# Performance work log

Measured on AMD Instinct MI355X. Metric: run time of the kernel, lower is better.

Reference implementation:

```python
import jax, jax.numpy as jnp
import numpy as np

B, L, DK, DV, H = 2, 2048, 512, 512, 8
DH_K = DK // H  # 64
DH_V = DV // H  # 64


def setup_inputs() -> dict:
    key = jax.random.key(0)
    ks = jax.random.split(key, 6)
    scale_w = 1.0 / np.sqrt(DK)
    return {
        "keys": jax.random.normal(ks[0], (B, L, DK), dtype=jnp.float32),
        "queries": jax.random.normal(ks[1], (B, L, DK), dtype=jnp.float32),
        "values": jax.random.normal(ks[2], (B, L, DV), dtype=jnp.float32),
        "WQ": jax.random.normal(ks[3], (H, DK, DH_K), dtype=jnp.float32) * scale_w,
        "WK": jax.random.normal(ks[4], (H, DK, DH_K), dtype=jnp.float32) * scale_w,
        "WV": jax.random.normal(ks[5], (H, DV, DH_V), dtype=jnp.float32) * scale_w,
    }


def reference(keys, queries, values, WQ, WK, WV):
    # Per-head projections, vectorized over all H heads at once.
    Q = jnp.einsum('bld,hde->bhle', queries, WQ)   # [B,H,Lq,dh]
    K = jnp.einsum('bld,hde->bhle', keys, WK)      # [B,H,Lk,dh]
    V = jnp.einsum('bld,hde->bhle', values, WV)    # [B,H,Lk,dv_h]
    Lk = keys.shape[1]
    # NOTE: original scales by sqrt(seq_len_k), not sqrt(head_dim).
    y = jnp.einsum('bhqe,bhke->bhqk', Q, K) / jnp.sqrt(jnp.float32(Lk))
    # NOTE: original applies softmax over torch dim=1 of [B,Lq,Lk],
    # i.e. the QUERY axis (axis=2 here in [B,H,Lq,Lk]).
    z = jax.nn.softmax(y, axis=2)
    out = jnp.einsum('bhqk,bhke->bhqe', z, V)      # [B,H,Lq,dv_h]
    # Concat heads on the feature dim (same order as torch.concat(..., 2)).
    Bq, Hh, Lq, Dh = out.shape
    return out.transpose(0, 2, 1, 3).reshape(Bq, Lq, Hh * Dh)
```

## Files before the change

### kernel.cpp

```cpp
#include <hip/hip_runtime.h>
#include <hip/hip_bf16.h>

#define LL 2048
#define DM 512
#define SCALE2 0.031879357f

typedef unsigned short u16;
typedef __attribute__((ext_vector_type(8))) short short8;
typedef __attribute__((ext_vector_type(4))) short short4v;
typedef __attribute__((ext_vector_type(4))) float f32x4;

#define XAQ_OFF 0u
#define XAK_OFF 2097152u
#define XAV_OFF 4194304u
#define WB_OFF  6291456u
#define QA_OFF  7077888u
#define KA_OFF  9175040u
#define VB_OFF  11272192u
#define S_OFF   13369344u

__device__ __forceinline__ u16 f2bf(float f) {
  union { float f; unsigned u; } v; v.f = f;
  unsigned r = v.u + 0x7fff + ((v.u >> 16) & 1);
  return (u16)(r >> 16);
}
__device__ __forceinline__ size_t frag_idx(int bh, int t64, int w, int c, int lane) {
  return ((((size_t)(bh * 32 + t64) * 4 + w) * 2 + c) * 64 + lane) * 8;
}
__device__ __forceinline__ size_t vb_idx(int bh, int kt, int w, int et, int lane) {
  return ((((size_t)(bh * 32 + kt) * 4 + w) * 4 + et) * 64 + lane) * 4;
}

__global__ __launch_bounds__(256) void prep_kernel(
    const float* __restrict__ queries, const float* __restrict__ keys,
    const float* __restrict__ values, const float* __restrict__ WQ,
    const float* __restrict__ WK, const float* __restrict__ WV,
    u16* __restrict__ wsb) {
  int t = threadIdx.x;
  int blk = blockIdx.x;
  if (blk < 768) {
    int tens = blk >> 8;
    int grp  = blk & 255;
    const float* src = (tens == 0 ? queries : tens == 1 ? keys : values) +
                       (size_t)grp * 16 * 512;
    __shared__ __align__(16) u16 Xs[16][520];
#pragma unroll
    for (int rep = 0; rep < 8; ++rep) {
      int f4 = t + rep * 256;
      int row = f4 >> 7, c4 = f4 & 127;
      float4 v = *(const float4*)(src + (size_t)row * 512 + c4 * 4);
      short4v o;
      o[0] = (short)f2bf(v.x); o[1] = (short)f2bf(v.y);
      o[2] = (short)f2bf(v.z); o[3] = (short)f2bf(v.w);
      *(short4v*)&Xs[row][c4 * 4] = o;
    }
    __syncthreads();
    u16* dst = wsb + (tens == 0 ? XAQ_OFF : tens == 1 ? XAK_OFF : XAV_OFF) +
               (size_t)grp * 16 * 64 * 8;
#pragma unroll
    for (int rep = 0; rep < 4; ++rep) {
      int o = t + rep * 256;
      int kt = o >> 6, lane = o & 63;
      int quad = lane >> 4, l16 = lane & 15;
      short8 v = *(const short8*)&Xs[l16][kt * 32 + quad * 8];
      *(short8*)(dst + (size_t)o * 8) = v;
    }
  } else {
    int c2 = (blk - 768) * 256 + t;
    int lane = c2 & 63;
    int nt = (c2 >> 6) & 3;
    int kt = (c2 >> 8) & 15;
    int h  = (c2 >> 12) & 7;
    int z  = c2 >> 15;
    int quad = lane >> 4, l16 = lane & 15;
    const float* W = (z == 0) ? WQ : (z == 1) ? WK : WV;
    const float* src = W + ((size_t)h * DM + kt * 32 + quad * 8) * 64 + nt * 16 + l16;
    short8 o;
#pragma unroll
    for (int j = 0; j < 8; ++j) o[j] = (short)f2bf(src[(size_t)j * 64]);
    *(short8*)(wsb + WB_OFF + (size_t)c2 * 8) = o;
  }
}

__global__ __launch_bounds__(256) void proj_kernel(u16* __restrict__ wsb) {
  int t = threadIdx.x;
  int lane = t & 63, w = t >> 6, quad = lane >> 4, l16 = lane & 15;
  int z = blockIdx.z, bh = blockIdx.y, b = bh >> 3, h = bh & 7;
  int QT = blockIdx.x;

  const u16* Bw = wsb + WB_OFF + ((size_t)(z * 8 + h) * 16) * 4 * 64 * 8;
  const u16* Ab = wsb + (z == 0 ? XAQ_OFF : z == 1 ? XAK_OFF : XAV_OFF) +
      (((size_t)b * 128 + QT * 4 + w) * 16) * 64 * 8;

  f32x4 acc[4];
#pragma unroll
  for (int nt = 0; nt < 4; ++nt) acc[nt] = (f32x4){0.f, 0.f, 0.f, 0.f};

#pragma unroll 4
  for (int kt = 0; kt < 16; ++kt) {
    short8 a = *(const short8*)(Ab + ((size_t)kt * 64 + lane) * 8);
#pragma unroll
    for (int nt = 0; nt < 4; ++nt) {
      short8 bb = *(const short8*)(Bw + (((size_t)kt * 4 + nt) * 64 + lane) * 8);
      acc[nt] = __builtin_amdgcn_mfma_f32_16x16x32_bf16(a, bb, acc[nt], 0, 0, 0);
    }
  }

  __shared__ float Cs[64][68];
  float sc = (z == 0) ? SCALE2 : 1.0f;
#pragma unroll
  for (int nt = 0; nt < 4; ++nt)
#pragma unroll
    for (int r = 0; r < 4; ++r)
      Cs[w * 16 + quad * 4 + r][nt * 16 + l16] = acc[nt][r] * sc;
  __syncthreads();

  if (z < 2) {
    u16* base = wsb + (z == 0 ? QA_OFF : KA_OFF);
#pragma unroll
    for (int c = 0; c < 2; ++c) {
      const float* srcr = &Cs[w * 16 + l16][c * 32 + quad * 8];
      short8 o;
#pragma unroll
      for (int j = 0; j < 8; ++j) o[j] = (short)f2bf(srcr[j]);
      *(short8*)(base + frag_idx(bh, QT, w, c, lane)) = o;
    }
  } else {
#pragma unroll
    for (int et = 0; et < 4; ++et) {
      short4v o;
#pragma unroll
      for (int j = 0; j < 4; ++j)
        o[j] = (short)f2bf(Cs[w * 16 + quad * 4 + j][et * 16 + l16]);
      *(short4v*)(wsb + VB_OFF + vb_idx(bh, QT, w, et, lane)) = o;
    }
  }
}

__global__ __launch_bounds__(256) void stats_kernel(u16* __restrict__ wsb) {
  int t = threadIdx.x;
  int lane = t & 63, w = t >> 6, quad = lane >> 4, l16 = lane & 15;
  int bh = blockIdx.x;
  int KT = blockIdx.y;

  short8 ka[4][2];
#pragma unroll
  for (int mt = 0; mt < 4; ++mt)
#pragma unroll
    for (int c = 0; c < 2; ++c)
      ka[mt][c] = *(const short8*)(wsb + KA_OFF + frag_idx(bh, KT, mt, c, lane));

  float rs[4][4];
#pragma unroll
  for (int mt = 0; mt < 4; ++mt)
#pragma unroll
    for (int r = 0; r < 4; ++r) rs[mt][r] = 0.f;

  short8 qb0 = *(const short8*)(wsb + QA_OFF + frag_idx(bh, 0, w, 0, lane));
  short8 qb1 = *(const short8*)(wsb + QA_OFF + frag_idx(bh, 0, w, 1, lane));
  for (int qt = 0; qt < 32; ++qt) {
    int qn = (qt + 1) & 31;
    short8 nq0 = *(const short8*)(wsb + QA_OFF + frag_idx(bh, qn, w, 0, lane));
    short8 nq1 = *(const short8*)(wsb + QA_OFF + frag_idx(bh, qn, w, 1, lane));
#pragma unroll
    for (int mt = 0; mt < 4; ++mt) {
      f32x4 y = (f32x4){0.f, 0.f, 0.f, 0.f};
      __builtin_amdgcn_s_setprio(1);
      y = __builtin_amdgcn_mfma_f32_16x16x32_bf16(ka[mt][0], qb0, y, 0, 0, 0);
      y = __builtin_amdgcn_mfma_f32_16x16x32_bf16(ka[mt][1], qb1, y, 0, 0, 0);
      __builtin_amdgcn_s_setprio(0);
#pragma unroll
      for (int r = 0; r < 4; ++r) rs[mt][r] += __builtin_amdgcn_exp2f(y[r]);
    }
    qb0 = nq0; qb1 = nq1;
  }
#pragma unroll
  for (int mt = 0; mt < 4; ++mt)
#pragma unroll
    for (int r = 0; r < 4; ++r) {
      rs[mt][r] += __shfl_xor(rs[mt][r], 1);
      rs[mt][r] += __shfl_xor(rs[mt][r], 2);
      rs[mt][r] += __shfl_xor(rs[mt][r], 4);
      rs[mt][r] += __shfl_xor(rs[mt][r], 8);
    }

  __shared__ float Sred[4][64];
  if (l16 == 0) {
#pragma unroll
    for (int mt = 0; mt < 4; ++mt)
#pragma unroll
      for (int r = 0; r < 4; ++r)
        Sred[w][mt * 16 + quad * 4 + r] = rs[mt][r];
  }
  __syncthreads();
  if (t < 64) {
    float s = Sred[0][t] + Sred[1][t] + Sred[2][t] + Sred[3][t];
    float* S = (float*)(wsb + S_OFF);
    S[(size_t)bh * LL + KT * 64 + t] = 1.0f / s;
  }
}

__global__ __launch_bounds__(256, 2) void attn_kernel(const u16* __restrict__ wsb,
                                                      float* __restrict__ out) {
  int t = threadIdx.x;
  int lane = t & 63, w = t >> 6, quad = lane >> 4, l16 = lane & 15;
  int bh = blockIdx.x, b = bh >> 3, h = bh & 7;
  int QT = blockIdx.y, qbase = QT * 64;
  const float* S = (const float*)(wsb + S_OFF) + (size_t)bh * LL;

  short8 qf[4][2];
#pragma unroll
  for (int nt = 0; nt < 4; ++nt)
#pragma unroll
    for (int c = 0; c < 2; ++c)
      qf[nt][c] = *(const short8*)(wsb + QA_OFF + frag_idx(bh, QT, nt, c, lane));

  f32x4 oacc[4][4];
#pragma unroll
  for (int nt = 0; nt < 4; ++nt)
#pragma unroll
    for (int et = 0; et < 4; ++et) oacc[nt][et] = (f32x4){0.f, 0.f, 0.f, 0.f};

  short8 ka0 = *(const short8*)(wsb + KA_OFF + frag_idx(bh, 0, w, 0, lane));
  short8 ka1 = *(const short8*)(wsb + KA_OFF + frag_idx(bh, 0, w, 1, lane));
  short4v vb[4];
#pragma unroll
  for (int et = 0; et < 4; ++et)
    vb[et] = *(const short4v*)(wsb + VB_OFF + vb_idx(bh, 0, w, et, lane));
  float4 s4 = *(const float4*)(S + w * 16 + quad * 4);

  for (int kt = 0; kt < 32; ++kt) {
    int kn = (kt + 1) & 31;
    short8 nka0 = *(const short8*)(wsb + KA_OFF + frag_idx(bh, kn, w, 0, lane));
    short8 nka1 = *(const short8*)(wsb + KA_OFF + frag_idx(bh, kn, w, 1, lane));
    short4v nvb[4];
#pragma unroll
    for (int et = 0; et < 4; ++et)
      nvb[et] = *(const short4v*)(wsb + VB_OFF + vb_idx(bh, kn, w, et, lane));
    float4 ns4 = *(const float4*)(S + kn * 64 + w * 16 + quad * 4);

#pragma unroll
    for (int nt = 0; nt < 4; ++nt) {
      f32x4 y = (f32x4){0.f, 0.f, 0.f, 0.f};
      __builtin_amdgcn_s_setprio(1);
      y = __builtin_amdgcn_mfma_f32_16x16x32_bf16(ka0, qf[nt][0], y, 0, 0, 0);
      y = __builtin_amdgcn_mfma_f32_16x16x32_bf16(ka1, qf[nt][1], y, 0, 0, 0);
      __builtin_amdgcn_s_setprio(0);
      float e0 = __builtin_amdgcn_exp2f(y[0]) * s4.x;
      float e1 = __builtin_amdgcn_exp2f(y[1]) * s4.y;
      float e2 = __builtin_amdgcn_exp2f(y[2]) * s4.z;
      float e3 = __builtin_amdgcn_exp2f(y[3]) * s4.w;
      short4v pa;
      pa[0] = (short)f2bf(e0);
      pa[1] = (short)f2bf(e1);
      pa[2] = (short)f2bf(e2);
      pa[3] = (short)f2bf(e3);
      __builtin_amdgcn_s_setprio(1);
#pragma unroll
      for (int et = 0; et < 4; ++et)
        oacc[nt][et] = __builtin_amdgcn_mfma_f32_16x16x16bf16_1k(pa, vb[et], oacc[nt][et], 0, 0, 0);
      __builtin_amdgcn_s_setprio(0);
    }
    ka0 = nka0; ka1 = nka1;
#pragma unroll
    for (int et = 0; et < 4; ++et) vb[et] = nvb[et];
    s4 = ns4;
  }

  __shared__ float red[4][64][68];
#pragma unroll
  for (int nt = 0; nt < 4; ++nt)
#pragma unroll
    for (int et = 0; et < 4; ++et)
#pragma unroll
      for (int r = 0; r < 4; ++r)
        red[w][nt * 16 + quad * 4 + r][et * 16 + l16] = oacc[nt][et][r];
  __syncthreads();
  float* og = out + ((size_t)b * LL + qbase + w * 16) * 512 + h * 64;
#pragma unroll
  for (int i = 0; i < 16; ++i) {
    float s = red[0][w * 16 + i][lane] + red[1][w * 16 + i][lane] +
              red[2][w * 16 + i][lane] + red[3][w * 16 + i][lane];
    og[(size_t)i * 512 + lane] = s;
  }
}

extern "C" void kernel_launch(void* const* d_in, const int* in_sizes, int n_in,
                              void* d_out, int out_size, void* d_ws, size_t ws_size,
                              hipStream_t stream) {
  const float* keys    = (const float*)d_in[0];
  const float* queries = (const float*)d_in[1];
  const float* values  = (const float*)d_in[2];
  const float* WQ      = (const float*)d_in[3];
  const float* WK      = (const float*)d_in[4];
  const float* WV      = (const float*)d_in[5];
  float* out = (float*)d_out;
  u16* wsb = (u16*)d_ws;

  prep_kernel<<<dim3(1152), 256, 0, stream>>>(queries, keys, values, WQ, WK, WV, wsb);
  proj_kernel<<<dim3(32, 16, 3), 256, 0, stream>>>(wsb);
  stats_kernel<<<dim3(16, 32), 256, 0, stream>>>(wsb);
  attn_kernel<<<dim3(16, 32), 256, 0, stream>>>(wsb, out);
}
```

Measured before the change: 138.1 us.

## Process key tiles in pairs to use K=32 MFMA for PV product

Changes the V fragment layout so two consecutive 64-key tiles are interleaved into 8-element bf16 fragments. The attention loop now handles two key tiles per iteration and packs both probability tiles into one short8 operand, so the PV product uses the 16x16x32 bf16 MFMA instead of two 16x16x16 ones. This halves the PV MFMA instruction count and the loop trip count, at the cost of more live registers for the doubled K/V/scale prefetch, which may reduce occupancy.

```diff
diff --git a/kernel.cpp b/kernel.cpp
--- a/kernel.cpp
+++ b/kernel.cpp
@@ -27,8 +27,8 @@
 __device__ __forceinline__ size_t frag_idx(int bh, int t64, int w, int c, int lane) {
   return ((((size_t)(bh * 32 + t64) * 4 + w) * 2 + c) * 64 + lane) * 8;
 }
-__device__ __forceinline__ size_t vb_idx(int bh, int kt, int w, int et, int lane) {
-  return ((((size_t)(bh * 32 + kt) * 4 + w) * 4 + et) * 64 + lane) * 4;
+__device__ __forceinline__ size_t vb8_idx(int bh, int kt2, int w, int et, int lane) {
+  return ((((size_t)(bh * 16 + kt2) * 4 + w) * 4 + et) * 64 + lane) * 8;
 }
 
 __global__ __launch_bounds__(256) void prep_kernel(
@@ -132,7 +132,7 @@
 #pragma unroll
       for (int j = 0; j < 4; ++j)
         o[j] = (short)f2bf(Cs[w * 16 + quad * 4 + j][et * 16 + l16]);
-      *(short4v*)(wsb + VB_OFF + vb_idx(bh, QT, w, et, lane)) = o;
+      *(short4v*)(wsb + VB_OFF + vb8_idx(bh, QT >> 1, w, et, lane) + (QT & 1) * 4) = o;
     }
   }
 }
@@ -221,50 +221,60 @@
 #pragma unroll
     for (int et = 0; et < 4; ++et) oacc[nt][et] = (f32x4){0.f, 0.f, 0.f, 0.f};
 
-  short8 ka0 = *(const short8*)(wsb + KA_OFF + frag_idx(bh, 0, w, 0, lane));
-  short8 ka1 = *(const short8*)(wsb + KA_OFF + frag_idx(bh, 0, w, 1, lane));
-  short4v vb[4];
+  short8 kae0 = *(const short8*)(wsb + KA_OFF + frag_idx(bh, 0, w, 0, lane));
+  short8 kae1 = *(const short8*)(wsb + KA_OFF + frag_idx(bh, 0, w, 1, lane));
+  short8 kao0 = *(const short8*)(wsb + KA_OFF + frag_idx(bh, 1, w, 0, lane));
+  short8 kao1 = *(const short8*)(wsb + KA_OFF + frag_idx(bh, 1, w, 1, lane));
+  short8 vb8[4];
 #pragma unroll
   for (int et = 0; et < 4; ++et)
-    vb[et] = *(const short4v*)(wsb + VB_OFF + vb_idx(bh, 0, w, et, lane));
-  float4 s4 = *(const float4*)(S + w * 16 + quad * 4);
-
-  for (int kt = 0; kt < 32; ++kt) {
-    int kn = (kt + 1) & 31;
-    short8 nka0 = *(const short8*)(wsb + KA_OFF + frag_idx(bh, kn, w, 0, lane));
-    short8 nka1 = *(const short8*)(wsb + KA_OFF + frag_idx(bh, kn, w, 1, lane));
-    short4v nvb[4];
+    vb8[et] = *(const short8*)(wsb + VB_OFF + vb8_idx(bh, 0, w, et, lane));
+  float4 s4e = *(const float4*)(S + 0 * 64 + w * 16 + quad * 4);
+  float4 s4o = *(const float4*)(S + 1 * 64 + w * 16 + quad * 4);
+
+  for (int kt2 = 0; kt2 < 16; ++kt2) {
+    int kne = (2 * kt2 + 2) & 31, kno = (2 * kt2 + 3) & 31;
+    int k2n = (kt2 + 1) & 15;
+    short8 nkae0 = *(const short8*)(wsb + KA_OFF + frag_idx(bh, kne, w, 0, lane));
+    short8 nkae1 = *(const short8*)(wsb + KA_OFF + frag_idx(bh, kne, w, 1, lane));
+    short8 nkao0 = *(const short8*)(wsb + KA_OFF + frag_idx(bh, kno, w, 0, lane));
+    short8 nkao1 = *(const short8*)(wsb + KA_OFF + frag_idx(bh, kno, w, 1, lane));
+    short8 nvb8[4];
 #pragma unroll
     for (int et = 0; et < 4; ++et)
-      nvb[et] = *(const short4v*)(wsb + VB_OFF + vb_idx(bh, kn, w, et, lane));
-    float4 ns4 = *(const float4*)(S + kn * 64 + w * 16 + quad * 4);
+      nvb8[et] = *(const short8*)(wsb + VB_OFF + vb8_idx(bh, k2n, w, et, lane));
+    float4 ns4e = *(const float4*)(S + kne * 64 + w * 16 + quad * 4);
+    float4 ns4o = *(const float4*)(S + kno * 64 + w * 16 + quad * 4);
 
 #pragma unroll
     for (int nt = 0; nt < 4; ++nt) {
-      f32x4 y = (f32x4){0.f, 0.f, 0.f, 0.f};
+      f32x4 ye = (f32x4){0.f, 0.f, 0.f, 0.f};
+      f32x4 yo = (f32x4){0.f, 0.f, 0.f, 0.f};
       __builtin_amdgcn_s_setprio(1);
-      y = __builtin_amdgcn_mfma_f32_16x16x32_bf16(ka0, qf[nt][0], y, 0, 0, 0);
-      y = __builtin_amdgcn_mfma_f32_16x16x32_bf16(ka1, qf[nt][1], y, 0, 0, 0);
+      ye = __builtin_amdgcn_mfma_f32_16x16x32_bf16(kae0, qf[nt][0], ye, 0, 0, 0);
+      ye = __builtin_amdgcn_mfma_f32_16x16x32_bf16(kae1, qf[nt][1], ye, 0, 0, 0);
+      yo = __builtin_amdgcn_mfma_f32_16x16x32_bf16(kao0, qf[nt][0], yo, 0, 0, 0);
+      yo = __builtin_amdgcn_mfma_f32_16x16x32_bf16(kao1, qf[nt][1], yo, 0, 0, 0);
       __builtin_amdgcn_s_setprio(0);
-      float e0 = __builtin_amdgcn_exp2f(y[0]) * s4.x;
-      float e1 = __builtin_amdgcn_exp2f(y[1]) * s4.y;
-      float e2 = __builtin_amdgcn_exp2f(y[2]) * s4.z;
-      float e3 = __builtin_amdgcn_exp2f(y[3]) * s4.w;
-      short4v pa;
-      pa[0] = (short)f2bf(e0);
-      pa[1] = (short)f2bf(e1);
-      pa[2] = (short)f2bf(e2);
-      pa[3] = (short)f2bf(e3);
+      short8 pa8;
+      pa8[0] = (short)f2bf(__builtin_amdgcn_exp2f(ye[0]) * s4e.x);
+      pa8[1] = (short)f2bf(__builtin_amdgcn_exp2f(ye[1]) * s4e.y);
+      pa8[2] = (short)f2bf(__builtin_amdgcn_exp2f(ye[2]) * s4e.z);
+      pa8[3] = (short)f2bf(__builtin_amdgcn_exp2f(ye[3]) * s4e.w);
+      pa8[4] = (short)f2bf(__builtin_amdgcn_exp2f(yo[0]) * s4o.x);
+      pa8[5] = (short)f2bf(__builtin_amdgcn_exp2f(yo[1]) * s4o.y);
+      pa8[6] = (short)f2bf(__builtin_amdgcn_exp2f(yo[2]) * s4o.z);
+      pa8[7] = (short)f2bf(__builtin_amdgcn_exp2f(yo[3]) * s4o.w);
       __builtin_amdgcn_s_setprio(1);
 #pragma unroll
       for (int et = 0; et < 4; ++et)
-        oacc[nt][et] = __builtin_amdgcn_mfma_f32_16x16x16bf16_1k(pa, vb[et], oacc[nt][et], 0, 0, 0);
+        oacc[nt][et] = __builtin_amdgcn_mfma_f32_16x16x32_bf16(pa8, vb8[et], oacc[nt][et], 0, 0, 0);
       __builtin_amdgcn_s_setprio(0);
     }
-    ka0 = nka0; ka1 = nka1;
-#pragma unroll
-    for (int et = 0; et < 4; ++et) vb[et] = nvb[et];
-    s4 = ns4;
+    kae0 = nkae0; kae1 = nkae1; kao0 = nkao0; kao1 = nkao1;
+#pragma unroll
+    for (int et = 0; et < 4; ++et) vb8[et] = nvb8[et];
+    s4e = ns4e; s4o = ns4o;
   }
 
   __shared__ float red[4][64][68];
```

Result: no change. 135.4 us (-1.9%).
